# Kernel optimization log

Hardware: AMD Instinct MI355X
Metric: run time of the kernel (lower is better)

## Reference

```python
import jax, jax.numpy as jnp
import numpy as np

NUM_EXPERTS = 8
TOP_K = 2
B, S, H = 4, 1024, 1024
FF = 2 * H  # expert hidden = 2*hidden_size per the torch code


def setup_inputs() -> dict:
    key = jax.random.key(0)
    ks = jax.random.split(key, 5)
    scale = 0.02
    return {
        "x": jax.random.normal(ks[0], (B, S, H), dtype=jnp.float32),
        "Wg": jax.random.normal(ks[1], (H, NUM_EXPERTS), dtype=jnp.float32) * scale,
        "bg": jnp.zeros((NUM_EXPERTS,), dtype=jnp.float32),
        "W1": jax.random.normal(ks[2], (NUM_EXPERTS, H, FF), dtype=jnp.float32) * scale,
        "b1": jnp.zeros((NUM_EXPERTS, FF), dtype=jnp.float32),
        "W2": jax.random.normal(ks[3], (NUM_EXPERTS, FF, H), dtype=jnp.float32) * scale,
        "b2": jnp.zeros((NUM_EXPERTS, H), dtype=jnp.float32),
    }


def reference(x, Wg, bg, W1, b1, W2, b2):
    b, s, h = x.shape
    xf = x.reshape(-1, h)  # [T, H]
    # Gating: softmax over experts, then top-k and renormalize (as in torch code)
    gate_scores = jax.nn.softmax(xf @ Wg + bg, axis=-1)  # [T, E]
    top_v, top_i = jax.lax.top_k(gate_scores, TOP_K)      # [T, K]
    top_v = top_v / jnp.sum(top_v, axis=-1, keepdims=True)
    # Combine weights per (token, expert): gate if expert selected else 0
    combine = jnp.sum(jax.nn.one_hot(top_i, NUM_EXPERTS, dtype=xf.dtype)
                      * top_v[..., None], axis=1)         # [T, E]
    # Dense all-expert MLP (eval-mode dropout = identity), then gated combine
    hmid = jax.nn.relu(jnp.einsum('th,ehf->tef', xf, W1) + b1)  # [T, E, FF]
    yexp = jnp.einsum('tef,efh->teh', hmid, W2) + b2            # [T, E, H]
    out = jnp.einsum('te,teh->th', combine, yexp)               # [T, H]
    return out.reshape(b, s, h)
```

## Files before the change

kernel.cpp:

```cpp
#include <hip/hip_runtime.h>
#include <hip/hip_bf16.h>

#define T_TOK 4096
#define HD    1024
#define FFD   2048
#define NE    8

typedef __attribute__((ext_vector_type(8))) short short8;
typedef __attribute__((ext_vector_type(4))) float f32x4;

__device__ __forceinline__ unsigned short f2bf(float f) {
  __hip_bfloat16 h = __float2bfloat16(f);
  return __builtin_bit_cast(unsigned short, h);
}

__device__ __forceinline__ void gload_lds16(const unsigned short* g, unsigned short* l) {
  __builtin_amdgcn_global_load_lds(
      (const __attribute__((address_space(1))) unsigned int*)g,
      (__attribute__((address_space(3))) unsigned int*)l, 16, 0, 0);
}

__global__ __launch_bounds__(256) void gate_kernel(
    const float* __restrict__ x, const float* __restrict__ Wg,
    const float* __restrict__ bg,
    int* __restrict__ top_i, float2* __restrict__ top_w,
    unsigned short* __restrict__ xbf, float* __restrict__ out)
{
  {
    size_t b = ((size_t)blockIdx.x * 256 + threadIdx.x) * 16;
    float4 z = make_float4(0.f, 0.f, 0.f, 0.f);
#pragma unroll
    for (int q = 0; q < 4; ++q) *(float4*)(out + b + q * 4) = z;
  }

  const int wave = threadIdx.x >> 6;
  const int lane = threadIdx.x & 63;
  const int t = blockIdx.x * 4 + wave;
  if (t >= T_TOK) return;

  float acc[NE];
#pragma unroll
  for (int e = 0; e < NE; ++e) acc[e] = 0.f;

  const float* xr = x + (size_t)t * HD;
  unsigned short* xo = xbf + (size_t)t * HD;
#pragma unroll
  for (int it = 0; it < 4; ++it) {
    const int h0 = lane * 4 + it * 256;
    float4 xv = *(const float4*)(xr + h0);
#pragma unroll
    for (int j = 0; j < 4; ++j) {
      float xs = (&xv.x)[j];
      float4 a = *(const float4*)(Wg + (size_t)(h0 + j) * NE);
      float4 b = *(const float4*)(Wg + (size_t)(h0 + j) * NE + 4);
      acc[0] = fmaf(xs, a.x, acc[0]); acc[1] = fmaf(xs, a.y, acc[1]);
      acc[2] = fmaf(xs, a.z, acc[2]); acc[3] = fmaf(xs, a.w, acc[3]);
      acc[4] = fmaf(xs, b.x, acc[4]); acc[5] = fmaf(xs, b.y, acc[5]);
      acc[6] = fmaf(xs, b.z, acc[6]); acc[7] = fmaf(xs, b.w, acc[7]);
    }
    ushort4 u;
    u.x = f2bf(xv.x); u.y = f2bf(xv.y); u.z = f2bf(xv.z); u.w = f2bf(xv.w);
    *(ushort4*)(xo + h0) = u;
  }
#pragma unroll
  for (int off = 32; off > 0; off >>= 1) {
#pragma unroll
    for (int e = 0; e < NE; ++e) acc[e] += __shfl_xor(acc[e], off);
  }
  if (lane == 0) {
    float lg[NE];
#pragma unroll
    for (int e = 0; e < NE; ++e) lg[e] = acc[e] + bg[e];
    int i1 = 0;
#pragma unroll
    for (int e = 1; e < NE; ++e) if (lg[e] > lg[i1]) i1 = e;
    int i2 = (i1 == 0) ? 1 : 0;
#pragma unroll
    for (int e = 0; e < NE; ++e) if (e != i1 && lg[e] > lg[i2]) i2 = e;
    float p2 = expf(lg[i2] - lg[i1]);
    float s  = 1.f + p2;
    top_i[t] = i1 | (i2 << 8);
    top_w[t] = make_float2(1.f / s, p2 / s);
  }
}

__global__ __launch_bounds__(256) void route_kernel(
    const int* __restrict__ top_i, const float2* __restrict__ top_w,
    int* __restrict__ counts, int* __restrict__ ids, float* __restrict__ wts)
{
  const int e   = blockIdx.x;
  const int tid = threadIdx.x;
  __shared__ int psum[256];

  const int t0 = tid * 16;
  unsigned int flags = 0;
  int cnt = 0;
#pragma unroll
  for (int j = 0; j < 16; ++j) {
    int ti = top_i[t0 + j];
    bool m = ((ti & 255) == e) || (((ti >> 8) & 255) == e);
    flags |= (m ? 1u : 0u) << j;
    cnt += m;
  }
  psum[tid] = cnt;
  __syncthreads();
  for (int off = 1; off < 256; off <<= 1) {
    int v = (tid >= off) ? psum[tid - off] : 0;
    __syncthreads();
    psum[tid] += v;
    __syncthreads();
  }
  int rank = psum[tid] - cnt;
#pragma unroll
  for (int j = 0; j < 16; ++j) {
    if (flags & (1u << j)) {
      int t = t0 + j;
      int ti = top_i[t];
      float2 w = top_w[t];
      ids[e * T_TOK + rank] = t;
      wts[e * T_TOK + rank] = ((ti & 255) == e) ? w.x : w.y;
      ++rank;
    }
  }
  if (tid == 255) counts[e] = psum[255];
}

__global__ __launch_bounds__(256) void transpose_cvt_kernel(
    const float* __restrict__ in, unsigned short* __restrict__ out,
    int R, int C)
{
  __shared__ float tile[64][69];
  const int z  = blockIdx.z;
  const int r0 = blockIdx.y * 64, c0 = blockIdx.x * 64;
  const int t  = threadIdx.x;
  const float* ip = in + ((size_t)z * R + r0) * C + c0;
  int tr = t >> 4, tc = (t & 15) * 4;
#pragma unroll
  for (int j = 0; j < 4; ++j) {
    float4 v = *(const float4*)(ip + (size_t)(tr + j * 16) * C + tc);
    float* tp = &tile[tr + j * 16][tc];
    tp[0] = v.x; tp[1] = v.y; tp[2] = v.z; tp[3] = v.w;
  }
  __syncthreads();
  unsigned short* op = out + ((size_t)z * C + c0) * R + r0;
  int oc = t >> 4, orr = (t & 15) * 4;
#pragma unroll
  for (int j = 0; j < 4; ++j) {
    int c = oc + j * 16;
    ushort4 w;
    w.x = f2bf(tile[orr + 0][c]);
    w.y = f2bf(tile[orr + 1][c]);
    w.z = f2bf(tile[orr + 2][c]);
    w.w = f2bf(tile[orr + 3][c]);
    *(ushort4*)(op + (size_t)c * R + orr) = w;
  }
}

template<int KD, int ND, bool G1M, bool GATHER_A>
__global__ __launch_bounds__(256, 4) void pair_gemm128_kernel(
    const unsigned short* __restrict__ A,
    const unsigned short* __restrict__ BT,
    const float* __restrict__ bias,
    const int* __restrict__ counts, const int* __restrict__ ids,
    const float* __restrict__ wts,
    unsigned short* __restrict__ Hout, float* __restrict__ out)
{
  constexpr int CT = ND / 128;

  const int e    = blockIdx.x & 7;
  const int slot = blockIdx.x >> 3;
  int cnt = 0, base = 0;
#pragma unroll
  for (int k = 0; k < NE; ++k) {
    int c = counts[k];
    if (k < e)  base += (c + 255) & ~255;
    if (k == e) cnt = c;
  }
  const int ntiles = (cnt + 127) >> 7;
  if (slot >= ntiles * CT) return;
  const int rt   = slot % ntiles;
  const int ct   = slot / ntiles;
  const int row0 = base + rt * 128;

  __shared__ __align__(16) unsigned short As[128 * 64];
  __shared__ __align__(16) unsigned short Bs[128 * 64];

  const int tid  = threadIdx.x;
  const int w    = tid >> 6;
  const int lane = tid & 63;
  const int g    = lane >> 4;
  const int rA   = lane & 15;
  const int wr   = w >> 1;
  const int wc   = w & 1;
  const int sw   = rA & 7;
  const int srow = lane >> 3;
  const int lc8  = ((lane & 7) ^ srow) * 8;

  const unsigned short* arow[4];
#pragma unroll
  for (int jj = 0; jj < 4; ++jj) {
    const int lrow = w * 32 + jj * 8 + srow;
    int src;
    if constexpr (GATHER_A) {
      int i = rt * 128 + lrow;
      src = ids[e * T_TOK + (i < cnt ? i : cnt - 1)];
    } else {
      src = row0 + lrow;
    }
    arow[jj] = A + (size_t)src * KD + lc8;
  }
  const unsigned short* Bb = BT + ((size_t)e * ND + (size_t)ct * 128) * KD + lc8;

  f32x4 acc[4][4];
#pragma unroll
  for (int mf = 0; mf < 4; ++mf)
#pragma unroll
    for (int nf = 0; nf < 4; ++nf)
      acc[mf][nf] = (f32x4){0.f, 0.f, 0.f, 0.f};

  for (int kc = 0; kc < KD; kc += 64) {
    __syncthreads();
#pragma unroll
    for (int jj = 0; jj < 4; ++jj) {
      const int rg = w * 32 + jj * 8;
      gload_lds16(arow[jj] + kc, &As[rg * 64]);
      gload_lds16(Bb + (size_t)(rg + srow) * KD + kc, &Bs[rg * 64]);
    }
    __syncthreads();
#pragma unroll
    for (int ks = 0; ks < 2; ++ks) {
      const int pc = ((ks * 4 + g) ^ sw) << 3;
      short8 af[4], bf[4];
#pragma unroll
      for (int mf = 0; mf < 4; ++mf)
        af[mf] = *(const short8*)&As[(wr * 64 + mf * 16 + rA) * 64 + pc];
#pragma unroll
      for (int nf = 0; nf < 4; ++nf)
        bf[nf] = *(const short8*)&Bs[(wc * 64 + nf * 16 + rA) * 64 + pc];
#pragma unroll
      for (int mf = 0; mf < 4; ++mf)
#pragma unroll
        for (int nf = 0; nf < 4; ++nf)
          acc[mf][nf] = __builtin_amdgcn_mfma_f32_16x16x32_bf16(
              af[mf], bf[nf], acc[mf][nf], 0, 0, 0);
    }
  }

  float bv[4];
#pragma unroll
  for (int nf = 0; nf < 4; ++nf)
    bv[nf] = bias[e * ND + ct * 128 + wc * 64 + nf * 16 + rA];

  if constexpr (G1M) {
#pragma unroll
    for (int mf = 0; mf < 4; ++mf)
#pragma unroll
      for (int r = 0; r < 4; ++r) {
        const int row = row0 + wr * 64 + mf * 16 + g * 4 + r;
        unsigned short* hrow = Hout + (size_t)row * FFD + ct * 128 + wc * 64 + rA;
#pragma unroll
        for (int nf = 0; nf < 4; ++nf)
          hrow[nf * 16] = f2bf(fmaxf(acc[mf][nf][r] + bv[nf], 0.f));
      }
  } else {
#pragma unroll
    for (int mf = 0; mf < 4; ++mf)
#pragma unroll
      for (int r = 0; r < 4; ++r) {
        const int i = rt * 128 + wr * 64 + mf * 16 + g * 4 + r;
        if (i >= cnt) continue;
        const int tok = ids[e * T_TOK + i];
        const float wt = wts[e * T_TOK + i];
        float* orow = out + (size_t)tok * HD + ct * 128 + wc * 64 + rA;
#pragma unroll
        for (int nf = 0; nf < 4; ++nf)
          atomicAdd(&orow[nf * 16], wt * (acc[mf][nf][r] + bv[nf]));
      }
  }
}

extern "C" void kernel_launch(void* const* d_in, const int* in_sizes, int n_in,
                              void* d_out, int out_size, void* d_ws, size_t ws_size,
                              hipStream_t stream) {
  const float* x  = (const float*)d_in[0];
  const float* Wg = (const float*)d_in[1];
  const float* bg = (const float*)d_in[2];
  const float* W1 = (const float*)d_in[3];
  const float* b1 = (const float*)d_in[4];
  const float* W2 = (const float*)d_in[5];
  const float* b2 = (const float*)d_in[6];
  float* out = (float*)d_out;

  const size_t OFF_TOPI = 512;
  const size_t OFF_TOPW = OFF_TOPI + (size_t)T_TOK * 4;
  const size_t OFF_IDS  = OFF_TOPW + (size_t)T_TOK * 8;
  const size_t OFF_WTS  = OFF_IDS + (size_t)T_TOK * NE * 4;
  const size_t OFF_XBF  = OFF_WTS + (size_t)T_TOK * NE * 4;
  const size_t OFF_WT   = OFF_XBF + (size_t)T_TOK * HD * 2;
  const size_t OFF_H    = OFF_WT + (size_t)NE * HD * FFD * 2;
  const size_t REQ      = OFF_H + (size_t)10240 * FFD * 2;

  if (ws_size < REQ) return;

  int*            counts = (int*)d_ws;
  int*            top_i  = (int*)((char*)d_ws + OFF_TOPI);
  float2*         top_w  = (float2*)((char*)d_ws + OFF_TOPW);
  int*            ids    = (int*)((char*)d_ws + OFF_IDS);
  float*          wts    = (float*)((char*)d_ws + OFF_WTS);
  unsigned short* xbf    = (unsigned short*)((char*)d_ws + OFF_XBF);
  unsigned short* WT     = (unsigned short*)((char*)d_ws + OFF_WT);
  unsigned short* H      = (unsigned short*)((char*)d_ws + OFF_H);

  gate_kernel<<<T_TOK / 4, 256, 0, stream>>>(x, Wg, bg, top_i, top_w, xbf, out);
  route_kernel<<<NE, 256, 0, stream>>>(top_i, top_w, counts, ids, wts);

  transpose_cvt_kernel<<<dim3(FFD / 64, HD / 64, NE), 256, 0, stream>>>(W1, WT, HD, FFD);
  pair_gemm128_kernel<HD, FFD, true, true>
      <<<NE * 512, 256, 0, stream>>>(xbf, WT, b1, counts, ids, wts, H, nullptr);

  transpose_cvt_kernel<<<dim3(HD / 64, FFD / 64, NE), 256, 0, stream>>>(W2, WT, FFD, HD);
  pair_gemm128_kernel<FFD, HD, false, false>
      <<<NE * 256, 256, 0, stream>>>(H, WT, b2, counts, ids, wts, nullptr, out);
}
```

Measured before the change: 175.2 us.

## Double-buffer LDS tiles in expert GEMM and split-K the second GEMM

Adds a two-stage LDS double buffer to the grouped expert GEMM, so the next K-chunk's global-to-LDS loads are issued before the current chunk's MFMAs, with explicit vmcnt waits and barriers. The second GEMM gets a split-K of 2, which doubles its grid; only the first K-part adds the bias, and the epilogue presumably accumulates into out atomically. The W1 and W2 transposes now use separate workspace buffers so both can run up front. In exchange, LDS use per block doubles, launch bounds drop to 2 blocks per SM, and the split-K adds more output write traffic.

```diff
diff --git a/kernel.cpp b/kernel.cpp
--- a/kernel.cpp
+++ b/kernel.cpp
@@ -156,8 +156,8 @@
   }
 }
 
-template<int KD, int ND, bool G1M, bool GATHER_A>
-__global__ __launch_bounds__(256, 4) void pair_gemm128_kernel(
+template<int KD, int ND, int KSPLIT, bool G1M, bool GATHER_A>
+__global__ __launch_bounds__(256, 2) void pair_gemm128_kernel(
     const unsigned short* __restrict__ A,
     const unsigned short* __restrict__ BT,
     const float* __restrict__ bias,
@@ -165,7 +165,9 @@
     const float* __restrict__ wts,
     unsigned short* __restrict__ Hout, float* __restrict__ out)
 {
-  constexpr int CT = ND / 128;
+  constexpr int CT    = ND / 128;
+  constexpr int KTILE = KD / KSPLIT;
+  constexpr int NT    = KTILE / 64;
 
   const int e    = blockIdx.x & 7;
   const int slot = blockIdx.x >> 3;
@@ -177,13 +179,15 @@
     if (k == e) cnt = c;
   }
   const int ntiles = (cnt + 127) >> 7;
-  if (slot >= ntiles * CT) return;
+  if (slot >= ntiles * CT * KSPLIT) return;
   const int rt   = slot % ntiles;
-  const int ct   = slot / ntiles;
+  const int ct   = (slot / ntiles) % CT;
+  const int kp   = slot / (ntiles * CT);
   const int row0 = base + rt * 128;
-
-  __shared__ __align__(16) unsigned short As[128 * 64];
-  __shared__ __align__(16) unsigned short Bs[128 * 64];
+  const int koff = kp * KTILE;
+
+  __shared__ __align__(16) unsigned short As[2][128 * 64];
+  __shared__ __align__(16) unsigned short Bs[2][128 * 64];
 
   const int tid  = threadIdx.x;
   const int w    = tid >> 6;
@@ -207,9 +211,9 @@
     } else {
       src = row0 + lrow;
     }
-    arow[jj] = A + (size_t)src * KD + lc8;
-  }
-  const unsigned short* Bb = BT + ((size_t)e * ND + (size_t)ct * 128) * KD + lc8;
+    arow[jj] = A + (size_t)src * KD + koff + lc8;
+  }
+  const unsigned short* Bb = BT + ((size_t)e * ND + (size_t)ct * 128) * KD + koff + lc8;
 
   f32x4 acc[4][4];
 #pragma unroll
@@ -218,25 +222,39 @@
     for (int nf = 0; nf < 4; ++nf)
       acc[mf][nf] = (f32x4){0.f, 0.f, 0.f, 0.f};
 
-  for (int kc = 0; kc < KD; kc += 64) {
-    __syncthreads();
+  auto stage = [&](int buf, int kc) {
 #pragma unroll
     for (int jj = 0; jj < 4; ++jj) {
       const int rg = w * 32 + jj * 8;
-      gload_lds16(arow[jj] + kc, &As[rg * 64]);
-      gload_lds16(Bb + (size_t)(rg + srow) * KD + kc, &Bs[rg * 64]);
-    }
-    __syncthreads();
+      gload_lds16(arow[jj] + kc, &As[buf][rg * 64]);
+      gload_lds16(Bb + (size_t)(rg + srow) * KD + kc, &Bs[buf][rg * 64]);
+    }
+  };
+
+  stage(0, 0);
+
+  for (int t = 0; t < NT; ++t) {
+    const int cur = t & 1;
+    if (t + 1 < NT) {
+      stage(cur ^ 1, (t + 1) * 64);
+      asm volatile("s_waitcnt vmcnt(8)" ::: "memory");
+    } else {
+      asm volatile("s_waitcnt vmcnt(0)" ::: "memory");
+    }
+    __builtin_amdgcn_sched_barrier(0);
+    __builtin_amdgcn_s_barrier();
+    __builtin_amdgcn_sched_barrier(0);
+
 #pragma unroll
     for (int ks = 0; ks < 2; ++ks) {
       const int pc = ((ks * 4 + g) ^ sw) << 3;
       short8 af[4], bf[4];
 #pragma unroll
       for (int mf = 0; mf < 4; ++mf)
-        af[mf] = *(const short8*)&As[(wr * 64 + mf * 16 + rA) * 64 + pc];
+        af[mf] = *(const short8*)&As[cur][(wr * 64 + mf * 16 + rA) * 64 + pc];
 #pragma unroll
       for (int nf = 0; nf < 4; ++nf)
-        bf[nf] = *(const short8*)&Bs[(wc * 64 + nf * 16 + rA) * 64 + pc];
+        bf[nf] = *(const short8*)&Bs[cur][(wc * 64 + nf * 16 + rA) * 64 + pc];
 #pragma unroll
       for (int mf = 0; mf < 4; ++mf)
 #pragma unroll
@@ -244,12 +262,18 @@
           acc[mf][nf] = __builtin_amdgcn_mfma_f32_16x16x32_bf16(
               af[mf], bf[nf], acc[mf][nf], 0, 0, 0);
     }
+
+    asm volatile("s_waitcnt lgkmcnt(0)" ::: "memory");
+    __builtin_amdgcn_sched_barrier(0);
+    __builtin_amdgcn_s_barrier();
+    __builtin_amdgcn_sched_barrier(0);
   }
 
   float bv[4];
 #pragma unroll
   for (int nf = 0; nf < 4; ++nf)
-    bv[nf] = bias[e * ND + ct * 128 + wc * 64 + nf * 16 + rA];
+    bv[nf] = (KSPLIT == 1 || kp == 0)
+                 ? bias[e * ND + ct * 128 + wc * 64 + nf * 16 + rA] : 0.f;
 
   if constexpr (G1M) {
 #pragma unroll
@@ -296,8 +320,9 @@
   const size_t OFF_IDS  = OFF_TOPW + (size_t)T_TOK * 8;
   const size_t OFF_WTS  = OFF_IDS + (size_t)T_TOK * NE * 4;
   const size_t OFF_XBF  = OFF_WTS + (size_t)T_TOK * NE * 4;
-  const size_t OFF_WT   = OFF_XBF + (size_t)T_TOK * HD * 2;
-  const size_t OFF_H    = OFF_WT + (size_t)NE * HD * FFD * 2;
+  const size_t OFF_W1T  = OFF_XBF + (size_t)T_TOK * HD * 2;
+  const size_t OFF_W2T  = OFF_W1T + (size_t)NE * HD * FFD * 2;
+  const size_t OFF_H    = OFF_W2T + (size_t)NE * HD * FFD * 2;
   const size_t REQ      = OFF_H + (size_t)10240 * FFD * 2;
 
   if (ws_size < REQ) return;
@@ -308,17 +333,17 @@
   int*            ids    = (int*)((char*)d_ws + OFF_IDS);
   float*          wts    = (float*)((char*)d_ws + OFF_WTS);
   unsigned short* xbf    = (unsigned short*)((char*)d_ws + OFF_XBF);
-  unsigned short* WT     = (unsigned short*)((char*)d_ws + OFF_WT);
+  unsigned short* W1T    = (unsigned short*)((char*)d_ws + OFF_W1T);
+  unsigned short* W2T    = (unsigned short*)((char*)d_ws + OFF_W2T);
   unsigned short* H      = (unsigned short*)((char*)d_ws + OFF_H);
 
   gate_kernel<<<T_TOK / 4, 256, 0, stream>>>(x, Wg, bg, top_i, top_w, xbf, out);
   route_kernel<<<NE, 256, 0, stream>>>(top_i, top_w, counts, ids, wts);
-
-  transpose_cvt_kernel<<<dim3(FFD / 64, HD / 64, NE), 256, 0, stream>>>(W1, WT, HD, FFD);
-  pair_gemm128_kernel<HD, FFD, true, true>
-      <<<NE * 512, 256, 0, stream>>>(xbf, WT, b1, counts, ids, wts, H, nullptr);
-
-  transpose_cvt_kernel<<<dim3(HD / 64, FFD / 64, NE), 256, 0, stream>>>(W2, WT, FFD, HD);
-  pair_gemm128_kernel<FFD, HD, false, false>
-      <<<NE * 256, 256, 0, stream>>>(H, WT, b2, counts, ids, wts, nullptr, out);
-}
+  transpose_cvt_kernel<<<dim3(FFD / 64, HD / 64, NE), 256, 0, stream>>>(W1, W1T, HD, FFD);
+  transpose_cvt_kernel<<<dim3(HD / 64, FFD / 64, NE), 256, 0, stream>>>(W2, W2T, FFD, HD);
+
+  pair_gemm128_kernel<HD, FFD, 1, true, true>
+      <<<NE * 512, 256, 0, stream>>>(xbf, W1T, b1, counts, ids, wts, H, nullptr);
+  pair_gemm128_kernel<FFD, HD, 2, false, false>
+      <<<NE * 512, 256, 0, stream>>>(H, W2T, b2, counts, ids, wts, nullptr, out);
+}
```

After: 225.1 us. 1.29x slower.

## Fuse gate and weight transposes into one prep kernel, persistent split-K GEMMs

Applied to the files above, without the earlier changes.

Merges the gating kernel and both weight transpose/convert kernels into a single launch. W1 and W2 now go into separate workspace buffers, which removes two launches and the serialization between them. Both expert GEMMs become persistent-style grids of 128 slots per expert that loop over jobs. The second GEMM splits K in two and accumulates through its existing atomics, with bias added only by the first split. The split doubles atomic traffic on the output and fixes the grid size independent of routing balance.

```diff
diff --git a/kernel.cpp b/kernel.cpp
--- a/kernel.cpp
+++ b/kernel.cpp
@@ -20,67 +20,109 @@
       (__attribute__((address_space(3))) unsigned int*)l, 16, 0, 0);
 }
 
-__global__ __launch_bounds__(256) void gate_kernel(
+__global__ __launch_bounds__(256) void prep_kernel(
     const float* __restrict__ x, const float* __restrict__ Wg,
     const float* __restrict__ bg,
+    const float* __restrict__ W1, const float* __restrict__ W2,
     int* __restrict__ top_i, float2* __restrict__ top_w,
-    unsigned short* __restrict__ xbf, float* __restrict__ out)
+    unsigned short* __restrict__ xbf,
+    unsigned short* __restrict__ W1T, unsigned short* __restrict__ W2T,
+    float* __restrict__ out)
 {
-  {
-    size_t b = ((size_t)blockIdx.x * 256 + threadIdx.x) * 16;
-    float4 z = make_float4(0.f, 0.f, 0.f, 0.f);
-#pragma unroll
-    for (int q = 0; q < 4; ++q) *(float4*)(out + b + q * 4) = z;
-  }
-
-  const int wave = threadIdx.x >> 6;
-  const int lane = threadIdx.x & 63;
-  const int t = blockIdx.x * 4 + wave;
-  if (t >= T_TOK) return;
-
-  float acc[NE];
-#pragma unroll
-  for (int e = 0; e < NE; ++e) acc[e] = 0.f;
-
-  const float* xr = x + (size_t)t * HD;
-  unsigned short* xo = xbf + (size_t)t * HD;
-#pragma unroll
-  for (int it = 0; it < 4; ++it) {
-    const int h0 = lane * 4 + it * 256;
-    float4 xv = *(const float4*)(xr + h0);
-#pragma unroll
-    for (int j = 0; j < 4; ++j) {
-      float xs = (&xv.x)[j];
-      float4 a = *(const float4*)(Wg + (size_t)(h0 + j) * NE);
-      float4 b = *(const float4*)(Wg + (size_t)(h0 + j) * NE + 4);
-      acc[0] = fmaf(xs, a.x, acc[0]); acc[1] = fmaf(xs, a.y, acc[1]);
-      acc[2] = fmaf(xs, a.z, acc[2]); acc[3] = fmaf(xs, a.w, acc[3]);
-      acc[4] = fmaf(xs, b.x, acc[4]); acc[5] = fmaf(xs, b.y, acc[5]);
-      acc[6] = fmaf(xs, b.z, acc[6]); acc[7] = fmaf(xs, b.w, acc[7]);
-    }
-    ushort4 u;
-    u.x = f2bf(xv.x); u.y = f2bf(xv.y); u.z = f2bf(xv.z); u.w = f2bf(xv.w);
-    *(ushort4*)(xo + h0) = u;
-  }
-#pragma unroll
-  for (int off = 32; off > 0; off >>= 1) {
-#pragma unroll
-    for (int e = 0; e < NE; ++e) acc[e] += __shfl_xor(acc[e], off);
-  }
-  if (lane == 0) {
-    float lg[NE];
-#pragma unroll
-    for (int e = 0; e < NE; ++e) lg[e] = acc[e] + bg[e];
-    int i1 = 0;
-#pragma unroll
-    for (int e = 1; e < NE; ++e) if (lg[e] > lg[i1]) i1 = e;
-    int i2 = (i1 == 0) ? 1 : 0;
-#pragma unroll
-    for (int e = 0; e < NE; ++e) if (e != i1 && lg[e] > lg[i2]) i2 = e;
-    float p2 = expf(lg[i2] - lg[i1]);
-    float s  = 1.f + p2;
-    top_i[t] = i1 | (i2 << 8);
-    top_w[t] = make_float2(1.f / s, p2 / s);
+  __shared__ float tile[64][69];
+  const int bid = blockIdx.x;
+  const int tid = threadIdx.x;
+
+  if (bid < T_TOK / 4) {
+    {
+      size_t b = ((size_t)bid * 256 + tid) * 16;
+      float4 z = make_float4(0.f, 0.f, 0.f, 0.f);
+#pragma unroll
+      for (int q = 0; q < 4; ++q) *(float4*)(out + b + q * 4) = z;
+    }
+    const int wave = tid >> 6;
+    const int lane = tid & 63;
+    const int t = bid * 4 + wave;
+
+    float acc[NE];
+#pragma unroll
+    for (int e = 0; e < NE; ++e) acc[e] = 0.f;
+
+    const float* xr = x + (size_t)t * HD;
+    unsigned short* xo = xbf + (size_t)t * HD;
+#pragma unroll
+    for (int it = 0; it < 4; ++it) {
+      const int h0 = lane * 4 + it * 256;
+      float4 xv = *(const float4*)(xr + h0);
+#pragma unroll
+      for (int j = 0; j < 4; ++j) {
+        float xs = (&xv.x)[j];
+        float4 a = *(const float4*)(Wg + (size_t)(h0 + j) * NE);
+        float4 b = *(const float4*)(Wg + (size_t)(h0 + j) * NE + 4);
+        acc[0] = fmaf(xs, a.x, acc[0]); acc[1] = fmaf(xs, a.y, acc[1]);
+        acc[2] = fmaf(xs, a.z, acc[2]); acc[3] = fmaf(xs, a.w, acc[3]);
+        acc[4] = fmaf(xs, b.x, acc[4]); acc[5] = fmaf(xs, b.y, acc[5]);
+        acc[6] = fmaf(xs, b.z, acc[6]); acc[7] = fmaf(xs, b.w, acc[7]);
+      }
+      ushort4 u;
+      u.x = f2bf(xv.x); u.y = f2bf(xv.y); u.z = f2bf(xv.z); u.w = f2bf(xv.w);
+      *(ushort4*)(xo + h0) = u;
+    }
+#pragma unroll
+    for (int off = 32; off > 0; off >>= 1) {
+#pragma unroll
+      for (int e = 0; e < NE; ++e) acc[e] += __shfl_xor(acc[e], off);
+    }
+    if (lane == 0) {
+      float lg[NE];
+#pragma unroll
+      for (int e = 0; e < NE; ++e) lg[e] = acc[e] + bg[e];
+      int i1 = 0;
+#pragma unroll
+      for (int e = 1; e < NE; ++e) if (lg[e] > lg[i1]) i1 = e;
+      int i2 = (i1 == 0) ? 1 : 0;
+#pragma unroll
+      for (int e = 0; e < NE; ++e) if (e != i1 && lg[e] > lg[i2]) i2 = e;
+      float p2 = expf(lg[i2] - lg[i1]);
+      float s  = 1.f + p2;
+      top_i[t] = i1 | (i2 << 8);
+      top_w[t] = make_float2(1.f / s, p2 / s);
+    }
+    return;
+  }
+
+  const float* in; unsigned short* ow; int R, C, idx;
+  if (bid < T_TOK / 4 + 4096) {
+    idx = bid - T_TOK / 4;          in = W1; ow = W1T; R = HD;  C = FFD;
+  } else {
+    idx = bid - (T_TOK / 4 + 4096); in = W2; ow = W2T; R = FFD; C = HD;
+  }
+  const int cpt = C >> 6, rpt = R >> 6;
+  const int cx = idx % cpt;
+  const int cy = (idx / cpt) % rpt;
+  const int z  = idx / (cpt * rpt);
+  const int r0 = cy * 64, c0 = cx * 64;
+
+  const float* ip = in + ((size_t)z * R + r0) * C + c0;
+  int tr = tid >> 4, tc = (tid & 15) * 4;
+#pragma unroll
+  for (int j = 0; j < 4; ++j) {
+    float4 v = *(const float4*)(ip + (size_t)(tr + j * 16) * C + tc);
+    float* tp = &tile[tr + j * 16][tc];
+    tp[0] = v.x; tp[1] = v.y; tp[2] = v.z; tp[3] = v.w;
+  }
+  __syncthreads();
+  unsigned short* op = ow + ((size_t)z * C + c0) * R + r0;
+  int oc = tid >> 4, orr = (tid & 15) * 4;
+#pragma unroll
+  for (int j = 0; j < 4; ++j) {
+    int c = oc + j * 16;
+    ushort4 w;
+    w.x = f2bf(tile[orr + 0][c]);
+    w.y = f2bf(tile[orr + 1][c]);
+    w.z = f2bf(tile[orr + 2][c]);
+    w.w = f2bf(tile[orr + 3][c]);
+    *(ushort4*)(op + (size_t)c * R + orr) = w;
   }
 }
 
@@ -125,38 +167,7 @@
   if (tid == 255) counts[e] = psum[255];
 }
 
-__global__ __launch_bounds__(256) void transpose_cvt_kernel(
-    const float* __restrict__ in, unsigned short* __restrict__ out,
-    int R, int C)
-{
-  __shared__ float tile[64][69];
-  const int z  = blockIdx.z;
-  const int r0 = blockIdx.y * 64, c0 = blockIdx.x * 64;
-  const int t  = threadIdx.x;
-  const float* ip = in + ((size_t)z * R + r0) * C + c0;
-  int tr = t >> 4, tc = (t & 15) * 4;
-#pragma unroll
-  for (int j = 0; j < 4; ++j) {
-    float4 v = *(const float4*)(ip + (size_t)(tr + j * 16) * C + tc);
-    float* tp = &tile[tr + j * 16][tc];
-    tp[0] = v.x; tp[1] = v.y; tp[2] = v.z; tp[3] = v.w;
-  }
-  __syncthreads();
-  unsigned short* op = out + ((size_t)z * C + c0) * R + r0;
-  int oc = t >> 4, orr = (t & 15) * 4;
-#pragma unroll
-  for (int j = 0; j < 4; ++j) {
-    int c = oc + j * 16;
-    ushort4 w;
-    w.x = f2bf(tile[orr + 0][c]);
-    w.y = f2bf(tile[orr + 1][c]);
-    w.z = f2bf(tile[orr + 2][c]);
-    w.w = f2bf(tile[orr + 3][c]);
-    *(ushort4*)(op + (size_t)c * R + orr) = w;
-  }
-}
-
-template<int KD, int ND, bool G1M, bool GATHER_A>
+template<int KD, int ND, int KSPLIT, bool G1M, bool GATHER_A>
 __global__ __launch_bounds__(256, 4) void pair_gemm128_kernel(
     const unsigned short* __restrict__ A,
     const unsigned short* __restrict__ BT,
@@ -165,10 +176,13 @@
     const float* __restrict__ wts,
     unsigned short* __restrict__ Hout, float* __restrict__ out)
 {
-  constexpr int CT = ND / 128;
-
-  const int e    = blockIdx.x & 7;
-  const int slot = blockIdx.x >> 3;
+  constexpr int CT    = ND / 128;
+  constexpr int KTILE = KD / KSPLIT;
+  constexpr int NT    = KTILE / 64;
+  constexpr int SPX   = 128;
+
+  const int e  = blockIdx.x & 7;
+  const int s0 = blockIdx.x >> 3;
   int cnt = 0, base = 0;
 #pragma unroll
   for (int k = 0; k < NE; ++k) {
@@ -177,10 +191,7 @@
     if (k == e) cnt = c;
   }
   const int ntiles = (cnt + 127) >> 7;
-  if (slot >= ntiles * CT) return;
-  const int rt   = slot % ntiles;
-  const int ct   = slot / ntiles;
-  const int row0 = base + rt * 128;
+  const int njobs  = ntiles * CT * KSPLIT;
 
   __shared__ __align__(16) unsigned short As[128 * 64];
   __shared__ __align__(16) unsigned short Bs[128 * 64];
@@ -196,86 +207,97 @@
   const int srow = lane >> 3;
   const int lc8  = ((lane & 7) ^ srow) * 8;
 
-  const unsigned short* arow[4];
-#pragma unroll
-  for (int jj = 0; jj < 4; ++jj) {
-    const int lrow = w * 32 + jj * 8 + srow;
-    int src;
-    if constexpr (GATHER_A) {
-      int i = rt * 128 + lrow;
-      src = ids[e * T_TOK + (i < cnt ? i : cnt - 1)];
+  for (int slot = s0; slot < njobs; slot += SPX) {
+    const int rt   = slot % ntiles;
+    const int ct   = (slot / ntiles) % CT;
+    const int kp   = slot / (ntiles * CT);
+    const int row0 = base + rt * 128;
+    const int koff = kp * KTILE;
+
+    const unsigned short* arow[4];
+#pragma unroll
+    for (int jj = 0; jj < 4; ++jj) {
+      const int lrow = w * 32 + jj * 8 + srow;
+      int src;
+      if constexpr (GATHER_A) {
+        int i = rt * 128 + lrow;
+        src = ids[e * T_TOK + (i < cnt ? i : cnt - 1)];
+      } else {
+        src = row0 + lrow;
+      }
+      arow[jj] = A + (size_t)src * KD + koff + lc8;
+    }
+    const unsigned short* Bb =
+        BT + ((size_t)e * ND + (size_t)ct * 128) * KD + koff + lc8;
+
+    f32x4 acc[4][4];
+#pragma unroll
+    for (int mf = 0; mf < 4; ++mf)
+#pragma unroll
+      for (int nf = 0; nf < 4; ++nf)
+        acc[mf][nf] = (f32x4){0.f, 0.f, 0.f, 0.f};
+
+    for (int kc = 0; kc < KTILE; kc += 64) {
+      __syncthreads();
+#pragma unroll
+      for (int jj = 0; jj < 4; ++jj) {
+        const int rg = w * 32 + jj * 8;
+        gload_lds16(arow[jj] + kc, &As[rg * 64]);
+        gload_lds16(Bb + (size_t)(rg + srow) * KD + kc, &Bs[rg * 64]);
+      }
+      __syncthreads();
+#pragma unroll
+      for (int ks = 0; ks < 2; ++ks) {
+        const int pc = ((ks * 4 + g) ^ sw) << 3;
+        short8 af[4], bf[4];
+#pragma unroll
+        for (int mf = 0; mf < 4; ++mf)
+          af[mf] = *(const short8*)&As[(wr * 64 + mf * 16 + rA) * 64 + pc];
+#pragma unroll
+        for (int nf = 0; nf < 4; ++nf)
+          bf[nf] = *(const short8*)&Bs[(wc * 64 + nf * 16 + rA) * 64 + pc];
+#pragma unroll
+        for (int mf = 0; mf < 4; ++mf)
+#pragma unroll
+          for (int nf = 0; nf < 4; ++nf)
+            acc[mf][nf] = __builtin_amdgcn_mfma_f32_16x16x32_bf16(
+                af[mf], bf[nf], acc[mf][nf], 0, 0, 0);
+      }
+    }
+
+    float bv[4];
+#pragma unroll
+    for (int nf = 0; nf < 4; ++nf)
+      bv[nf] = (KSPLIT == 1 || kp == 0)
+                   ? bias[e * ND + ct * 128 + wc * 64 + nf * 16 + rA] : 0.f;
+
+    if constexpr (G1M) {
+#pragma unroll
+      for (int mf = 0; mf < 4; ++mf)
+#pragma unroll
+        for (int r = 0; r < 4; ++r) {
+          const int row = row0 + wr * 64 + mf * 16 + g * 4 + r;
+          unsigned short* hrow =
+              Hout + (size_t)row * FFD + ct * 128 + wc * 64 + rA;
+#pragma unroll
+          for (int nf = 0; nf < 4; ++nf)
+            hrow[nf * 16] = f2bf(fmaxf(acc[mf][nf][r] + bv[nf], 0.f));
+        }
     } else {
-      src = row0 + lrow;
-    }
-    arow[jj] = A + (size_t)src * KD + lc8;
-  }
-  const unsigned short* Bb = BT + ((size_t)e * ND + (size_t)ct * 128) * KD + lc8;
-
-  f32x4 acc[4][4];
-#pragma unroll
-  for (int mf = 0; mf < 4; ++mf)
-#pragma unroll
-    for (int nf = 0; nf < 4; ++nf)
-      acc[mf][nf] = (f32x4){0.f, 0.f, 0.f, 0.f};
-
-  for (int kc = 0; kc < KD; kc += 64) {
-    __syncthreads();
-#pragma unroll
-    for (int jj = 0; jj < 4; ++jj) {
-      const int rg = w * 32 + jj * 8;
-      gload_lds16(arow[jj] + kc, &As[rg * 64]);
-      gload_lds16(Bb + (size_t)(rg + srow) * KD + kc, &Bs[rg * 64]);
-    }
-    __syncthreads();
-#pragma unroll
-    for (int ks = 0; ks < 2; ++ks) {
-      const int pc = ((ks * 4 + g) ^ sw) << 3;
-      short8 af[4], bf[4];
 #pragma unroll
       for (int mf = 0; mf < 4; ++mf)
-        af[mf] = *(const short8*)&As[(wr * 64 + mf * 16 + rA) * 64 + pc];
-#pragma unroll
-      for (int nf = 0; nf < 4; ++nf)
-        bf[nf] = *(const short8*)&Bs[(wc * 64 + nf * 16 + rA) * 64 + pc];
-#pragma unroll
-      for (int mf = 0; mf < 4; ++mf)
-#pragma unroll
-        for (int nf = 0; nf < 4; ++nf)
-          acc[mf][nf] = __builtin_amdgcn_mfma_f32_16x16x32_bf16(
-              af[mf], bf[nf], acc[mf][nf], 0, 0, 0);
-    }
-  }
-
-  float bv[4];
-#pragma unroll
-  for (int nf = 0; nf < 4; ++nf)
-    bv[nf] = bias[e * ND + ct * 128 + wc * 64 + nf * 16 + rA];
-
-  if constexpr (G1M) {
-#pragma unroll
-    for (int mf = 0; mf < 4; ++mf)
-#pragma unroll
-      for (int r = 0; r < 4; ++r) {
-        const int row = row0 + wr * 64 + mf * 16 + g * 4 + r;
-        unsigned short* hrow = Hout + (size_t)row * FFD + ct * 128 + wc * 64 + rA;
-#pragma unroll
-        for (int nf = 0; nf < 4; ++nf)
-          hrow[nf * 16] = f2bf(fmaxf(acc[mf][nf][r] + bv[nf], 0.f));
-      }
-  } else {
-#pragma unroll
-    for (int mf = 0; mf < 4; ++mf)
-#pragma unroll
-      for (int r = 0; r < 4; ++r) {
-        const int i = rt * 128 + wr * 64 + mf * 16 + g * 4 + r;
-        if (i >= cnt) continue;
-        const int tok = ids[e * T_TOK + i];
-        const float wt = wts[e * T_TOK + i];
-        float* orow = out + (size_t)tok * HD + ct * 128 + wc * 64 + rA;
-#pragma unroll
-        for (int nf = 0; nf < 4; ++nf)
-          atomicAdd(&orow[nf * 16], wt * (acc[mf][nf][r] + bv[nf]));
-      }
+#pragma unroll
+        for (int r = 0; r < 4; ++r) {
+          const int i = rt * 128 + wr * 64 + mf * 16 + g * 4 + r;
+          if (i >= cnt) continue;
+          const int tok = ids[e * T_TOK + i];
+          const float wt = wts[e * T_TOK + i];
+          float* orow = out + (size_t)tok * HD + ct * 128 + wc * 64 + rA;
+#pragma unroll
+          for (int nf = 0; nf < 4; ++nf)
+            atomicAdd(&orow[nf * 16], wt * (acc[mf][nf][r] + bv[nf]));
+        }
+    }
   }
 }
 
@@ -296,8 +318,9 @@
   const size_t OFF_IDS  = OFF_TOPW + (size_t)T_TOK * 8;
   const size_t OFF_WTS  = OFF_IDS + (size_t)T_TOK * NE * 4;
   const size_t OFF_XBF  = OFF_WTS + (size_t)T_TOK * NE * 4;
-  const size_t OFF_WT   = OFF_XBF + (size_t)T_TOK * HD * 2;
-  const size_t OFF_H    = OFF_WT + (size_t)NE * HD * FFD * 2;
+  const size_t OFF_W1T  = OFF_XBF + (size_t)T_TOK * HD * 2;
+  const size_t OFF_W2T  = OFF_W1T + (size_t)NE * HD * FFD * 2;
+  const size_t OFF_H    = OFF_W2T + (size_t)NE * HD * FFD * 2;
   const size_t REQ      = OFF_H + (size_t)10240 * FFD * 2;
 
   if (ws_size < REQ) return;
@@ -308,17 +331,16 @@
   int*            ids    = (int*)((char*)d_ws + OFF_IDS);
   float*          wts    = (float*)((char*)d_ws + OFF_WTS);
   unsigned short* xbf    = (unsigned short*)((char*)d_ws + OFF_XBF);
-  unsigned short* WT     = (unsigned short*)((char*)d_ws + OFF_WT);
+  unsigned short* W1T    = (unsigned short*)((char*)d_ws + OFF_W1T);
+  unsigned short* W2T    = (unsigned short*)((char*)d_ws + OFF_W2T);
   unsigned short* H      = (unsigned short*)((char*)d_ws + OFF_H);
 
-  gate_kernel<<<T_TOK / 4, 256, 0, stream>>>(x, Wg, bg, top_i, top_w, xbf, out);
+  prep_kernel<<<T_TOK / 4 + 2 * 4096, 256, 0, stream>>>(
+      x, Wg, bg, W1, W2, top_i, top_w, xbf, W1T, W2T, out);
   route_kernel<<<NE, 256, 0, stream>>>(top_i, top_w, counts, ids, wts);
 
-  transpose_cvt_kernel<<<dim3(FFD / 64, HD / 64, NE), 256, 0, stream>>>(W1, WT, HD, FFD);
-  pair_gemm128_kernel<HD, FFD, true, true>
-      <<<NE * 512, 256, 0, stream>>>(xbf, WT, b1, counts, ids, wts, H, nullptr);
-
-  transpose_cvt_kernel<<<dim3(HD / 64, FFD / 64, NE), 256, 0, stream>>>(W2, WT, FFD, HD);
-  pair_gemm128_kernel<FFD, HD, false, false>
-      <<<NE * 256, 256, 0, stream>>>(H, WT, b2, counts, ids, wts, nullptr, out);
-}
+  pair_gemm128_kernel<HD, FFD, 1, true, true>
+      <<<NE * 128, 256, 0, stream>>>(xbf, W1T, b1, counts, ids, wts, H, nullptr);
+  pair_gemm128_kernel<FFD, HD, 2, false, false>
+      <<<NE * 128, 256, 0, stream>>>(H, W2T, b2, counts, ids, wts, nullptr, out);
+}
```

Result: slower. 192.2 us (+9.7%).
